# Kernel tuning notes

Measured on AMD Instinct MI355X. Metric: run time of the kernel, lower is better.

## Reference

```python
import jax, jax.numpy as jnp
import numpy as np

IN_SIZE = 256
HIDDEN = 512
T = 32768


def setup_inputs() -> dict:
    key = jax.random.key(0)
    ks = jax.random.split(key, 6)
    lim_ih = 1.0 / np.sqrt(HIDDEN)
    inp = {
        "input": jax.random.normal(ks[0], (T, IN_SIZE), dtype=jnp.float32),
        "init_hidden": jax.random.normal(ks[1], (HIDDEN,), dtype=jnp.float32),
        # eqx.nn.GRUCell parameters: weight_ih (3H, in), weight_hh (3H, H), bias (3H,), bias_n (H,)
        "weight_ih": jax.random.uniform(ks[2], (3 * HIDDEN, IN_SIZE), minval=-lim_ih, maxval=lim_ih, dtype=jnp.float32),
        "weight_hh": jax.random.uniform(ks[3], (3 * HIDDEN, HIDDEN), minval=-lim_ih, maxval=lim_ih, dtype=jnp.float32),
        "bias": jax.random.uniform(ks[4], (3 * HIDDEN,), minval=-lim_ih, maxval=lim_ih, dtype=jnp.float32),
        "bias_n": jax.random.uniform(ks[5], (HIDDEN,), minval=-lim_ih, maxval=lim_ih, dtype=jnp.float32),
    }
    return inp


def reference(input, init_hidden, weight_ih, weight_hh, bias, bias_n):
    H = init_hidden.shape[0]
    # Precompute all input-side gates in one big GEMM: [T, 3H]
    igates_all = input @ weight_ih.T + bias

    def step(h, ig):
        hg = weight_hh @ h  # [3H]
        ir, iz, inn = ig[:H], ig[H:2 * H], ig[2 * H:]
        hr, hz, hn = hg[:H], hg[H:2 * H], hg[2 * H:]
        reset = jax.nn.sigmoid(ir + hr)
        upd = jax.nn.sigmoid(iz + hz)
        new = jnp.tanh(inn + reset * (hn + bias_n))
        h_new = new + upd * (h - new)
        # rnn_out_o = atleast_2d(h_new) -> (1, H); [..., 0] -> (1,)
        return h_new, h_new[:1]

    _, out = jax.lax.scan(step, init_hidden, igates_all)
    return out  # [T, 1]
```

## Files before the change

### kernel.cpp

```cpp
#include <hip/hip_runtime.h>


#define T_STEPS    32768
#define INSZ       256
#define HSZ        512
#define TPB        512
#define NWG        16
#define SWG        32
#define POLL_GUARD 16384

typedef unsigned long long u64;
typedef unsigned int u32;
typedef u32 u32x4 __attribute__((ext_vector_type(4)));
typedef float f32x4 __attribute__((ext_vector_type(4)));
typedef float f32x2 __attribute__((ext_vector_type(2)));

__device__ __forceinline__ float grp_reduce16(float v) {
  v += __shfl_xor(v, 1);
  v += __shfl_xor(v, 2);
  v += __shfl_xor(v, 4);
  v += __shfl_xor(v, 8);
  return v;
}

__device__ __forceinline__ int hpad(int k) { return k + 4 * (k >> 5); }

__device__ __forceinline__ void st16_sys(u64* p, u32x4 v) {
  asm volatile("global_store_dwordx4 %0, %1, off sc0 sc1" :: "v"(p), "v"(v) : "memory");
}

__global__ void init_comm(u64* __restrict__ comm, const float* __restrict__ h0) {
  int jj = threadIdx.x;
  u32 bits = __float_as_uint(h0[jj]);
  comm[jj]       = (u64)bits;
  comm[HSZ + jj] = 0xFFFFFFFF00000000ull;
}

__launch_bounds__(TPB, 2)
__global__ void gru_persistent(const float* __restrict__ input,
                               const float* __restrict__ w_ih,
                               const float* __restrict__ w_hh,
                               const float* __restrict__ bias,
                               const float* __restrict__ bias_n,
                               u64* __restrict__ comm,
                               float* __restrict__ out)
{
  const int tid = threadIdx.x;
  const int wg  = blockIdx.x;
  const int g   = tid >> 4;
  const int l   = tid & 15;
  const int laneid = tid & 63;
  const int j   = wg * SWG + g;

  f32x4 whh[3][8];
  f32x4 wih[3][4];
  #pragma unroll
  for (int q = 0; q < 3; ++q) {
    const float* rp = w_hh + (size_t)(j + 512 * q) * HSZ + l * 32;
    #pragma unroll
    for (int c = 0; c < 8; ++c) whh[q][c] = *(const f32x4*)(rp + c * 4);
    const float* rp2 = w_ih + (size_t)(j + 512 * q) * INSZ + l * 16;
    #pragma unroll
    for (int c = 0; c < 4; ++c) wih[q][c] = *(const f32x4*)(rp2 + c * 4);
  }
  const float b_r = bias[j], b_z = bias[j + 512], b_n = bias[j + 1024];
  const float bn2 = bias_n[j];

  __shared__ float h_lds[2][HSZ + 4 * (HSZ >> 5)];

  float ig0, ig1, ig2;
  {
    const float* ip = input + l * 16;
    float a0 = 0.f, a1 = 0.f, a2 = 0.f;
    #pragma unroll
    for (int c = 0; c < 4; ++c) {
      f32x4 xv = *(const f32x4*)(ip + c * 4);
      #pragma unroll
      for (int u = 0; u < 4; ++u) {
        a0 += wih[0][c][u] * xv[u];
        a1 += wih[1][c][u] * xv[u];
        a2 += wih[2][c][u] * xv[u];
      }
    }
    ig0 = grp_reduce16(a0); ig1 = grp_reduce16(a1); ig2 = grp_reduce16(a2);
  }

#define ISSUE(R) \
  asm volatile("global_load_dwordx4 %0, %1, off sc0 sc1" : "=&v"(R) : "v"(lp) : "memory")
#define CHECK(R) \
  asm volatile("s_waitcnt vmcnt(3)" : "+v"(R)); \
  __builtin_amdgcn_sched_barrier(0); \
  if ((R[1] == tt && R[3] == tt) || --guard == 0) { win = R; break; } \
  ISSUE(R)

  for (int t = 0; t < T_STEPS; ++t) {
    asm volatile("" :
      "+v"(whh[0][0]), "+v"(whh[0][1]), "+v"(whh[0][2]), "+v"(whh[0][3]),
      "+v"(whh[0][4]), "+v"(whh[0][5]), "+v"(whh[0][6]), "+v"(whh[0][7]),
      "+v"(whh[1][0]), "+v"(whh[1][1]), "+v"(whh[1][2]), "+v"(whh[1][3]),
      "+v"(whh[1][4]), "+v"(whh[1][5]), "+v"(whh[1][6]), "+v"(whh[1][7]),
      "+v"(whh[2][0]), "+v"(whh[2][1]), "+v"(whh[2][2]), "+v"(whh[2][3]),
      "+v"(whh[2][4]), "+v"(whh[2][5]), "+v"(whh[2][6]), "+v"(whh[2][7]));
    asm volatile("" :
      "+v"(wih[0][0]), "+v"(wih[0][1]), "+v"(wih[0][2]), "+v"(wih[0][3]),
      "+v"(wih[1][0]), "+v"(wih[1][1]), "+v"(wih[1][2]), "+v"(wih[1][3]),
      "+v"(wih[2][0]), "+v"(wih[2][1]), "+v"(wih[2][2]), "+v"(wih[2][3]));

    const int p  = t & 1;
    const u32 tt = (u32)t;

    if (tid < 256) {
      const u64* lp = comm + (size_t)p * HSZ + 2 * tid;
      u32x4 a, b, c, d, win;
      asm volatile("s_waitcnt vmcnt(0)" ::: "memory");
      ISSUE(a); ISSUE(b); ISSUE(c); ISSUE(d);
      int guard = POLL_GUARD;
      for (;;) {
        CHECK(a);
        CHECK(b);
        CHECK(c);
        CHECK(d);
      }
      asm volatile("s_waitcnt vmcnt(0)" : "+v"(a), "+v"(b), "+v"(c), "+v"(d));
      __builtin_amdgcn_sched_barrier(0);
      f32x2 hv2;
      hv2[0] = __uint_as_float(win[0]);
      hv2[1] = __uint_as_float(win[2]);
      *(f32x2*)&h_lds[p][hpad(2 * tid)] = hv2;
    }
    __syncthreads();

    const int tn = (t + 1 < T_STEPS) ? (t + 1) : (T_STEPS - 1);
    const float* ipn = input + (size_t)tn * INSZ + l * 16;
    f32x4 nv0 = *(const f32x4*)(ipn + 0);
    f32x4 nv1 = *(const f32x4*)(ipn + 4);
    f32x4 nv2 = *(const f32x4*)(ipn + 8);
    f32x4 nv3 = *(const f32x4*)(ipn + 12);

    float hr = 0.f, hz = 0.f, hn = 0.f;
    const float* hp = &h_lds[p][l * 36];
    #pragma unroll
    for (int c = 0; c < 8; ++c) {
      f32x4 hv = *(const f32x4*)(hp + c * 4);
      #pragma unroll
      for (int u = 0; u < 4; ++u) {
        hr += whh[0][c][u] * hv[u];
        hz += whh[1][c][u] * hv[u];
        hn += whh[2][c][u] * hv[u];
      }
    }
    hr = grp_reduce16(hr); hz = grp_reduce16(hz); hn = grp_reduce16(hn);

    const float reset = 1.0f / (1.0f + __expf(-(ig0 + b_r + hr)));
    const float upd   = 1.0f / (1.0f + __expf(-(ig1 + b_z + hz)));
    const float hold  = h_lds[p][hpad(j)];
    const float newv  = tanhf(ig2 + b_n + reset * (hn + bn2));
    const float hnew  = newv + upd * (hold - newv);

    const float hpart = __shfl(hnew, (laneid + 16) & 63);
    if (l == 0 && (g & 1) == 0) {
      u64* nbuf = comm + (size_t)((t + 1) & 1) * HSZ;
      u32x4 pk;
      pk[0] = __float_as_uint(hnew);  pk[1] = (u32)(t + 1);
      pk[2] = __float_as_uint(hpart); pk[3] = (u32)(t + 1);
      st16_sys(&nbuf[j], pk);
      if (j == 0) out[t] = hnew;
    }

    {
      float a0 = 0.f, a1 = 0.f, a2 = 0.f;
      #pragma unroll
      for (int c = 0; c < 4; ++c) {
        f32x4 xv = (c == 0) ? nv0 : ((c == 1) ? nv1 : ((c == 2) ? nv2 : nv3));
        #pragma unroll
        for (int u = 0; u < 4; ++u) {
          a0 += wih[0][c][u] * xv[u];
          a1 += wih[1][c][u] * xv[u];
          a2 += wih[2][c][u] * xv[u];
        }
      }
      ig0 = grp_reduce16(a0); ig1 = grp_reduce16(a1); ig2 = grp_reduce16(a2);
    }
  }
#undef ISSUE
#undef CHECK
}

extern "C" void kernel_launch(void* const* d_in, const int* in_sizes, int n_in,
                              void* d_out, int out_size, void* d_ws, size_t ws_size,
                              hipStream_t stream) {
  const float* input  = (const float*)d_in[0];
  const float* h0     = (const float*)d_in[1];
  const float* w_ih   = (const float*)d_in[2];
  const float* w_hh   = (const float*)d_in[3];
  const float* bias   = (const float*)d_in[4];
  const float* bias_n = (const float*)d_in[5];
  float* out = (float*)d_out;
  u64* comm  = (u64*)d_ws;

  hipLaunchKernelGGL(init_comm, dim3(1), dim3(HSZ), 0, stream, comm, h0);
  hipLaunchKernelGGL(gru_persistent, dim3(NWG), dim3(TPB), 0, stream,
                     input, w_ih, w_hh, bias, bias_n, comm, out);
}
```

Measured before the change: 62.67 ms.

## Split GRU rows across 32 workgroups with one gate row per thread group

```diff
diff --git a/kernel.cpp b/kernel.cpp
--- a/kernel.cpp
+++ b/kernel.cpp
@@ -4,9 +4,8 @@
 #define T_STEPS    32768
 #define INSZ       256
 #define HSZ        512
-#define TPB        512
-#define NWG        16
-#define SWG        32
+#define TPB        768
+#define NWG        32
 #define POLL_GUARD 16384
 
 typedef unsigned long long u64;
@@ -36,8 +35,9 @@
   comm[HSZ + jj] = 0xFFFFFFFF00000000ull;
 }
 
-__launch_bounds__(TPB, 2)
+__launch_bounds__(TPB, 1)
 __global__ void gru_persistent(const float* __restrict__ input,
+                               const float* __restrict__ init_hidden,
                                const float* __restrict__ w_ih,
                                const float* __restrict__ w_hh,
                                const float* __restrict__ bias,
@@ -49,137 +49,135 @@
   const int wg  = blockIdx.x;
   const int g   = tid >> 4;
   const int l   = tid & 15;
-  const int laneid = tid & 63;
-  const int j   = wg * SWG + g;
-
-  f32x4 whh[3][8];
-  f32x4 wih[3][4];
-  #pragma unroll
-  for (int q = 0; q < 3; ++q) {
-    const float* rp = w_hh + (size_t)(j + 512 * q) * HSZ + l * 32;
+  const int R   = wg * 16 + (g & 15) + 512 * (g >> 4);
+
+  f32x4 whh[8];
+  f32x4 wih[4];
+  {
+    const float* rp = w_hh + (size_t)R * HSZ + l * 32;
     #pragma unroll
-    for (int c = 0; c < 8; ++c) whh[q][c] = *(const f32x4*)(rp + c * 4);
-    const float* rp2 = w_ih + (size_t)(j + 512 * q) * INSZ + l * 16;
+    for (int c = 0; c < 8; ++c) whh[c] = *(const f32x4*)(rp + c * 4);
+    const float* rp2 = w_ih + (size_t)R * INSZ + l * 16;
     #pragma unroll
-    for (int c = 0; c < 4; ++c) wih[q][c] = *(const f32x4*)(rp2 + c * 4);
-  }
-  const float b_r = bias[j], b_z = bias[j + 512], b_n = bias[j + 1024];
-  const float bn2 = bias_n[j];
+    for (int c = 0; c < 4; ++c) wih[c] = *(const f32x4*)(rp2 + c * 4);
+  }
+
+  float hold = 0.f, b_r = 0.f, b_z = 0.f, b_n = 0.f, bn = 0.f;
+  if (tid < 16) {
+    const int j = wg * 16 + tid;
+    hold = init_hidden[j];
+    b_r  = bias[j];
+    b_z  = bias[j + 512];
+    b_n  = bias[j + 1024];
+    bn   = bias_n[j];
+  }
 
   __shared__ float h_lds[2][HSZ + 4 * (HSZ >> 5)];
-
-  float ig0, ig1, ig2;
+  __shared__ float gsum[48];
+  __shared__ float isum[2][48];
+  __shared__ float xstage[INSZ];
+
+  if (tid < 64) {
+    f32x4 v = *(const f32x4*)(input + tid * 4);
+    *(f32x4*)&xstage[tid * 4] = v;
+  }
+  __syncthreads();
   {
-    const float* ip = input + l * 16;
-    float a0 = 0.f, a1 = 0.f, a2 = 0.f;
+    float a = 0.f;
     #pragma unroll
     for (int c = 0; c < 4; ++c) {
-      f32x4 xv = *(const f32x4*)(ip + c * 4);
+      f32x4 xv = *(const f32x4*)&xstage[l * 16 + c * 4];
       #pragma unroll
-      for (int u = 0; u < 4; ++u) {
-        a0 += wih[0][c][u] * xv[u];
-        a1 += wih[1][c][u] * xv[u];
-        a2 += wih[2][c][u] * xv[u];
-      }
-    }
-    ig0 = grp_reduce16(a0); ig1 = grp_reduce16(a1); ig2 = grp_reduce16(a2);
-  }
-
-#define ISSUE(R) \
-  asm volatile("global_load_dwordx4 %0, %1, off sc0 sc1" : "=&v"(R) : "v"(lp) : "memory")
-#define CHECK(R) \
-  asm volatile("s_waitcnt vmcnt(3)" : "+v"(R)); \
+      for (int u = 0; u < 4; ++u) a += wih[c][u] * xv[u];
+    }
+    a = grp_reduce16(a);
+    if (l == 0) isum[0][g] = a;
+  }
+
+  const int poller = (tid >= 256 && tid < 512);
+  const int pt     = tid - 256;
+  const int stager = (tid >= 512 && tid < 576);
+  u32x4 pa, pb, pc, pd, win;
+
+#define ISSUE(Rr) \
+  asm volatile("global_load_dwordx4 %0, %1, off sc0 sc1" : "=&v"(Rr) : "v"(lp) : "memory")
+#define CHECK(Rr) \
+  asm volatile("s_waitcnt vmcnt(3)" : "+v"(Rr)); \
   __builtin_amdgcn_sched_barrier(0); \
-  if ((R[1] == tt && R[3] == tt) || --guard == 0) { win = R; break; } \
-  ISSUE(R)
+  if ((Rr[1] == tt && Rr[3] == tt) || --guard == 0) { win = Rr; break; } \
+  ISSUE(Rr)
 
   for (int t = 0; t < T_STEPS; ++t) {
-    asm volatile("" :
-      "+v"(whh[0][0]), "+v"(whh[0][1]), "+v"(whh[0][2]), "+v"(whh[0][3]),
-      "+v"(whh[0][4]), "+v"(whh[0][5]), "+v"(whh[0][6]), "+v"(whh[0][7]),
-      "+v"(whh[1][0]), "+v"(whh[1][1]), "+v"(whh[1][2]), "+v"(whh[1][3]),
-      "+v"(whh[1][4]), "+v"(whh[1][5]), "+v"(whh[1][6]), "+v"(whh[1][7]),
-      "+v"(whh[2][0]), "+v"(whh[2][1]), "+v"(whh[2][2]), "+v"(whh[2][3]),
-      "+v"(whh[2][4]), "+v"(whh[2][5]), "+v"(whh[2][6]), "+v"(whh[2][7]));
-    asm volatile("" :
-      "+v"(wih[0][0]), "+v"(wih[0][1]), "+v"(wih[0][2]), "+v"(wih[0][3]),
-      "+v"(wih[1][0]), "+v"(wih[1][1]), "+v"(wih[1][2]), "+v"(wih[1][3]),
-      "+v"(wih[2][0]), "+v"(wih[2][1]), "+v"(wih[2][2]), "+v"(wih[2][3]));
-
     const int p  = t & 1;
     const u32 tt = (u32)t;
 
-    if (tid < 256) {
-      const u64* lp = comm + (size_t)p * HSZ + 2 * tid;
-      u32x4 a, b, c, d, win;
-      asm volatile("s_waitcnt vmcnt(0)" ::: "memory");
-      ISSUE(a); ISSUE(b); ISSUE(c); ISSUE(d);
+    if (poller) {
+      const u64* lp = comm + (size_t)p * HSZ + 2 * pt;
+      ISSUE(pa); ISSUE(pb); ISSUE(pc); ISSUE(pd);
       int guard = POLL_GUARD;
       for (;;) {
-        CHECK(a);
-        CHECK(b);
-        CHECK(c);
-        CHECK(d);
-      }
-      asm volatile("s_waitcnt vmcnt(0)" : "+v"(a), "+v"(b), "+v"(c), "+v"(d));
-      __builtin_amdgcn_sched_barrier(0);
-      f32x2 hv2;
-      hv2[0] = __uint_as_float(win[0]);
-      hv2[1] = __uint_as_float(win[2]);
-      *(f32x2*)&h_lds[p][hpad(2 * tid)] = hv2;
+        CHECK(pa);
+        CHECK(pb);
+        CHECK(pc);
+        CHECK(pd);
+      }
+      f32x2 hv;
+      hv[0] = __uint_as_float(win[0]);
+      hv[1] = __uint_as_float(win[2]);
+      *(f32x2*)&h_lds[p][hpad(2 * pt)] = hv;
+    }
+    f32x4 xnew = {0.f, 0.f, 0.f, 0.f};
+    if (stager) {
+      const int tn = (t + 1 < T_STEPS) ? (t + 1) : (T_STEPS - 1);
+      xnew = *(const f32x4*)(input + (size_t)tn * INSZ + (tid - 512) * 4);
     }
     __syncthreads();
 
-    const int tn = (t + 1 < T_STEPS) ? (t + 1) : (T_STEPS - 1);
-    const float* ipn = input + (size_t)tn * INSZ + l * 16;
-    f32x4 nv0 = *(const f32x4*)(ipn + 0);
-    f32x4 nv1 = *(const f32x4*)(ipn + 4);
-    f32x4 nv2 = *(const f32x4*)(ipn + 8);
-    f32x4 nv3 = *(const f32x4*)(ipn + 12);
-
-    float hr = 0.f, hz = 0.f, hn = 0.f;
-    const float* hp = &h_lds[p][l * 36];
-    #pragma unroll
-    for (int c = 0; c < 8; ++c) {
-      f32x4 hv = *(const f32x4*)(hp + c * 4);
+    float a = 0.f;
+    {
+      const float* hp = &h_lds[p][l * 36];
       #pragma unroll
-      for (int u = 0; u < 4; ++u) {
-        hr += whh[0][c][u] * hv[u];
-        hz += whh[1][c][u] * hv[u];
-        hn += whh[2][c][u] * hv[u];
-      }
-    }
-    hr = grp_reduce16(hr); hz = grp_reduce16(hz); hn = grp_reduce16(hn);
-
-    const float reset = 1.0f / (1.0f + __expf(-(ig0 + b_r + hr)));
-    const float upd   = 1.0f / (1.0f + __expf(-(ig1 + b_z + hz)));
-    const float hold  = h_lds[p][hpad(j)];
-    const float newv  = tanhf(ig2 + b_n + reset * (hn + bn2));
-    const float hnew  = newv + upd * (hold - newv);
-
-    const float hpart = __shfl(hnew, (laneid + 16) & 63);
-    if (l == 0 && (g & 1) == 0) {
-      u64* nbuf = comm + (size_t)((t + 1) & 1) * HSZ;
-      u32x4 pk;
-      pk[0] = __float_as_uint(hnew);  pk[1] = (u32)(t + 1);
-      pk[2] = __float_as_uint(hpart); pk[3] = (u32)(t + 1);
-      st16_sys(&nbuf[j], pk);
-      if (j == 0) out[t] = hnew;
+      for (int c = 0; c < 8; ++c) {
+        f32x4 hv4 = *(const f32x4*)(hp + c * 4);
+        #pragma unroll
+        for (int u = 0; u < 4; ++u) a += whh[c][u] * hv4[u];
+      }
+    }
+    a = grp_reduce16(a);
+    if (l == 0) gsum[g] = a;
+    if (stager) *(f32x4*)&xstage[(tid - 512) * 4] = xnew;
+    __syncthreads();
+
+    if (tid < 16) {
+      const int j = tid;
+      const float hr = gsum[j], hz = gsum[16 + j], hn = gsum[32 + j];
+      const float i_r = isum[p][j], i_z = isum[p][16 + j], i_n = isum[p][32 + j];
+      const float reset = 1.0f / (1.0f + __expf(-(i_r + b_r + hr)));
+      const float upd   = 1.0f / (1.0f + __expf(-(i_z + b_z + hz)));
+      const float newv  = tanhf(i_n + b_n + reset * (hn + bn));
+      const float hnew  = newv + upd * (hold - newv);
+      hold = hnew;
+      const float hpair = __shfl(hnew, tid + 1);
+      if ((j & 1) == 0) {
+        u64* nbuf = comm + (size_t)((t + 1) & 1) * HSZ;
+        u32x4 pk;
+        pk[0] = __float_as_uint(hnew);  pk[1] = (u32)(t + 1);
+        pk[2] = __float_as_uint(hpair); pk[3] = (u32)(t + 1);
+        st16_sys(&nbuf[wg * 16 + j], pk);
+        if (wg == 0 && j == 0) out[t] = hnew;
+      }
     }
 
     {
-      float a0 = 0.f, a1 = 0.f, a2 = 0.f;
+      float a2 = 0.f;
       #pragma unroll
       for (int c = 0; c < 4; ++c) {
-        f32x4 xv = (c == 0) ? nv0 : ((c == 1) ? nv1 : ((c == 2) ? nv2 : nv3));
+        f32x4 xv = *(const f32x4*)&xstage[l * 16 + c * 4];
         #pragma unroll
-        for (int u = 0; u < 4; ++u) {
-          a0 += wih[0][c][u] * xv[u];
-          a1 += wih[1][c][u] * xv[u];
-          a2 += wih[2][c][u] * xv[u];
-        }
-      }
-      ig0 = grp_reduce16(a0); ig1 = grp_reduce16(a1); ig2 = grp_reduce16(a2);
+        for (int u = 0; u < 4; ++u) a2 += wih[c][u] * xv[u];
+      }
+      a2 = grp_reduce16(a2);
+      if (l == 0) isum[(t + 1) & 1][g] = a2;
     }
   }
 #undef ISSUE
@@ -200,5 +198,5 @@
 
   hipLaunchKernelGGL(init_comm, dim3(1), dim3(HSZ), 0, stream, comm, h0);
   hipLaunchKernelGGL(gru_persistent, dim3(NWG), dim3(TPB), 0, stream,
-                     input, w_ih, w_hh, bias, bias_n, comm, out);
-}
+                     input, h0, w_ih, w_hh, bias, bias_n, comm, out);
+}
```

New measurement: 57.91 ms. 1.08x faster.
